# Kernel optimization log

Measured on AMD Instinct MI355X. Metric: run time of the kernel, lower is better.

Reference implementation:

```python
import jax, jax.numpy as jnp
import numpy as np

VOCAB = 32000
TIME = 4096
EMBED = 512
B, T = 4, 4096


def setup_inputs() -> dict:
    key = jax.random.key(0)
    k1, k2, k3 = jax.random.split(key, 3)
    x = jax.random.randint(k1, (B, T), 0, VOCAB, dtype=jnp.int64 if jax.config.jax_enable_x64 else jnp.int32)
    tok_weight = jax.random.normal(k2, (VOCAB, EMBED), dtype=jnp.float32)
    pos_weight = jax.random.normal(k3, (TIME, EMBED), dtype=jnp.float32)
    return {"x": x, "tok_weight": tok_weight, "pos_weight": pos_weight}


def reference(x, tok_weight, pos_weight):
    # one_hot(x) @ W is mathematically a row gather: W[x]
    seq_len = x.shape[1]
    tok = jnp.take(tok_weight, x, axis=0)                 # [B, T, E]
    pos = jax.lax.dynamic_slice_in_dim(pos_weight, 0, seq_len, axis=0)  # [T, E]
    return tok + pos[None, :, :]
```

## Files before the change

kernel.cpp:

```cpp
#include <hip/hip_runtime.h>
#include <hip/hip_bf16.h>


#define TT 4096
#define EV4 128

__global__ __launch_bounds__(256) void pos_embed_kernel(
    const int* __restrict__ x,
    const float4* __restrict__ tok_w,
    const float4* __restrict__ pos_w,
    float4* __restrict__ out,
    int n4)
{
    int idx = blockIdx.x * blockDim.x + threadIdx.x;
    if (idx >= n4) return;

    int row  = idx >> 7;
    int col4 = idx & (EV4 - 1);
    int t    = row & (TT - 1);

    int tok_row = x[row];

    float4 a = tok_w[(size_t)tok_row * EV4 + col4];
    float4 p = pos_w[(size_t)t * EV4 + col4];

    float4 r;
    r.x = a.x + p.x;
    r.y = a.y + p.y;
    r.z = a.z + p.z;
    r.w = a.w + p.w;

    out[idx] = r;
}

extern "C" void kernel_launch(void* const* d_in, const int* in_sizes, int n_in,
                              void* d_out, int out_size, void* d_ws, size_t ws_size,
                              hipStream_t stream) {
    const int*    x     = (const int*)d_in[0];
    const float4* tok_w = (const float4*)d_in[1];
    const float4* pos_w = (const float4*)d_in[2];
    float4*       out   = (float4*)d_out;

    int n4 = out_size / 4;
    int block = 256;
    int grid  = (n4 + block - 1) / block;

    pos_embed_kernel<<<grid, block, 0, stream>>>(x, tok_w, pos_w, out, n4);
}
```

Baseline: 110.0 us.

## Map one wavefront per row with scalar token index and nontemporal stores

Each 64-lane wavefront now handles a full 512-float embedding row, issuing two float4 loads per table per lane. The token index is made wave-uniform with readfirstlane, and results are written with nontemporal stores so the output stream does not displace cached table data. This removes the per-thread redundant index loads and divide/mod work. In exchange there are fewer threads in flight, and the grid is sized as nrows/4 with no tail handling.

```diff
diff --git a/kernel.cpp b/kernel.cpp
--- a/kernel.cpp
+++ b/kernel.cpp
@@ -5,32 +5,37 @@
 #define TT 4096
 #define EV4 128
 
+typedef float f32x4 __attribute__((ext_vector_type(4)));
+
 __global__ __launch_bounds__(256) void pos_embed_kernel(
     const int* __restrict__ x,
     const float4* __restrict__ tok_w,
     const float4* __restrict__ pos_w,
     float4* __restrict__ out,
-    int n4)
+    int nrows)
 {
-    int idx = blockIdx.x * blockDim.x + threadIdx.x;
-    if (idx >= n4) return;
+    const int lane = threadIdx.x & 63;
+    const int wave = threadIdx.x >> 6;
+    const int row  = blockIdx.x * 4 + wave;
+    if (row >= nrows) return;
 
-    int row  = idx >> 7;
-    int col4 = idx & (EV4 - 1);
-    int t    = row & (TT - 1);
+    const int t = row & (TT - 1);
+    const int tok_row = __builtin_amdgcn_readfirstlane(x[row]);
 
-    int tok_row = x[row];
+    const float4* ta = tok_w + (size_t)tok_row * EV4;
+    const float4* pa = pos_w + (size_t)t * EV4;
+    float4*       oa = out   + (size_t)row * EV4;
 
-    float4 a = tok_w[(size_t)tok_row * EV4 + col4];
-    float4 p = pos_w[(size_t)t * EV4 + col4];
+    float4 a0 = ta[lane];
+    float4 a1 = ta[lane + 64];
+    float4 p0 = pa[lane];
+    float4 p1 = pa[lane + 64];
 
-    float4 r;
-    r.x = a.x + p.x;
-    r.y = a.y + p.y;
-    r.z = a.z + p.z;
-    r.w = a.w + p.w;
+    f32x4 r0 = {a0.x + p0.x, a0.y + p0.y, a0.z + p0.z, a0.w + p0.w};
+    f32x4 r1 = {a1.x + p1.x, a1.y + p1.y, a1.z + p1.z, a1.w + p1.w};
 
-    out[idx] = r;
+    __builtin_nontemporal_store(r0, (f32x4*)&oa[lane]);
+    __builtin_nontemporal_store(r1, (f32x4*)&oa[lane + 64]);
 }
 
 extern "C" void kernel_launch(void* const* d_in, const int* in_sizes, int n_in,
@@ -41,9 +46,9 @@
     const float4* pos_w = (const float4*)d_in[2];
     float4*       out   = (float4*)d_out;
 
-    int n4 = out_size / 4;
+    int nrows = out_size / 512;
     int block = 256;
-    int grid  = (n4 + block - 1) / block;
+    int grid  = nrows / 4;
 
-    pos_embed_kernel<<<grid, block, 0, stream>>>(x, tok_w, pos_w, out, n4);
+    pos_embed_kernel<<<grid, block, 0, stream>>>(x, tok_w, pos_w, out, nrows);
 }
```

After: 111.9 us. No clear change (+1.7%).
